# Kernel optimization log

Measured on AMD Instinct MI355X. Metric: run time of the kernel, lower is better.

Reference implementation:

```python
import jax, jax.numpy as jnp
import numpy as np

DIM = 1024
NQ = 16
NKV = 4
HD = DIM // NQ  # 64
HID = 2048
E = 8
B, S = 1, 1024
EPS = 1e-6


def rmsnorm(x, w):
    ms = jnp.mean(x * x, axis=-1, keepdims=True)
    return w * (x * jax.lax.rsqrt(ms + EPS))


def rope_tables(seq_len, head_dim):
    inv_freq = 1.0 / (10000.0 ** (jnp.arange(0, head_dim, 2, dtype=jnp.float32) / head_dim))
    t = jnp.arange(seq_len, dtype=jnp.float32)
    freqs = jnp.einsum('i,j->ij', t, inv_freq)  # [S, HD/2]
    return jnp.cos(freqs), jnp.sin(freqs)


def apply_rope(x, cos, sin):
    # x: [B, S, H, HD]; cos/sin: [S, HD/2]
    c = cos[None, :, None, :]
    s = sin[None, :, None, :]
    half = x.shape[-1] // 2
    x1, x2 = x[..., :half], x[..., half:]
    return jnp.concatenate([x1 * c - x2 * s, x1 * s + x2 * c], axis=-1)


def setup_inputs() -> dict:
    key = jax.random.key(0)
    ks = jax.random.split(key, 20)
    sc = lambda fan_in: 1.0 / np.sqrt(fan_in)
    d = {}
    d['x'] = jax.random.normal(ks[0], (B, S, DIM), dtype=jnp.float32)
    d['ln1_w'] = jnp.ones((DIM,), jnp.float32)
    d['ln2_w'] = jnp.ones((DIM,), jnp.float32)
    d['Wq'] = jax.random.normal(ks[1], (DIM, DIM), jnp.float32) * sc(DIM)
    d['bq'] = jnp.zeros((DIM,), jnp.float32)
    d['Wk'] = jax.random.normal(ks[2], (DIM, HD * NKV), jnp.float32) * sc(DIM)
    d['bk'] = jnp.zeros((HD * NKV,), jnp.float32)
    d['Wv'] = jax.random.normal(ks[3], (DIM, HD * NKV), jnp.float32) * sc(DIM)
    d['bv'] = jnp.zeros((HD * NKV,), jnp.float32)
    d['qn_w'] = jnp.ones((HD,), jnp.float32)
    d['kn_w'] = jnp.ones((HD,), jnp.float32)
    d['Wg'] = jax.random.normal(ks[4], (HD, HD), jnp.float32) * sc(HD)
    d['bg'] = jnp.zeros((HD,), jnp.float32)
    d['Wo'] = jax.random.normal(ks[5], (DIM, DIM), jnp.float32) * sc(DIM)
    d['bo'] = jnp.zeros((DIM,), jnp.float32)
    d['Wr'] = jax.random.normal(ks[6], (DIM, E), jnp.float32) * sc(DIM)
    d['br'] = jnp.zeros((E,), jnp.float32)
    d['W1'] = jax.random.normal(ks[7], (E, DIM, 2 * HID), jnp.float32) * sc(DIM)
    d['b1'] = jnp.zeros((E, 2 * HID), jnp.float32)
    d['W2'] = jax.random.normal(ks[8], (E, HID, DIM), jnp.float32) * sc(HID)
    d['b2'] = jnp.zeros((E, DIM), jnp.float32)
    return d


def _forward(x, ln1_w, ln2_w, Wq, bq, Wk, bk, Wv, bv, qn_w, kn_w, Wg, bg, Wo, bo,
             Wr, br, W1, b1, W2, b2):
    batch, seq, _ = x.shape
    cos, sin = rope_tables(seq, HD)

    # --- attention ---
    h = rmsnorm(x, ln1_w)
    q = (h @ Wq + bq).reshape(batch, seq, NQ, HD)
    k = (h @ Wk + bk).reshape(batch, seq, NKV, HD)
    v = (h @ Wv + bv).reshape(batch, seq, NKV, HD)
    q = rmsnorm(apply_rope(q, cos, sin), qn_w)
    k = rmsnorm(apply_rope(k, cos, sin), kn_w)
    rep = NQ // NKV
    k = jnp.repeat(k, rep, axis=2)  # [B,S,NQ,HD]
    v = jnp.repeat(v, rep, axis=2)
    scores = jnp.einsum('bthd,bshd->bhts', q, k) / np.sqrt(HD)
    causal = jnp.tril(jnp.ones((seq, seq), dtype=bool))
    scores = jnp.where(causal[None, None], scores, -jnp.inf)
    attn = jax.nn.softmax(scores, axis=-1)
    out = jnp.einsum('bhts,bshd->bthd', attn, v)
    gate = jax.nn.sigmoid(out @ Wg + bg)
    out = (out * gate).reshape(batch, seq, DIM)
    x = x + out @ Wo + bo

    # --- top-1 MoE (note: output is NOT scaled by router probs) ---
    h2 = rmsnorm(x, ln2_w)
    logits = h2 @ Wr + br  # [B,S,E]
    top1 = jnp.argmax(logits, axis=-1).reshape(-1)  # [T]
    xt = h2.reshape(-1, DIM)  # [T,DIM]
    # dense dispatch: run all experts, gather the chosen one
    u = jnp.einsum('td,edf->tef', xt, W1) + b1  # [T,E,2H]
    u1, u2 = u[..., :HID], u[..., HID:]
    act = u1 * jax.nn.sigmoid(u2)  # SwiGLU
    y_all = jnp.einsum('teh,ehd->ted', act, W2) + b2  # [T,E,DIM]
    y = jnp.take_along_axis(y_all, top1[:, None, None], axis=1)[:, 0, :]
    return x + y.reshape(batch, seq, DIM)


def reference(x, ln1_w, ln2_w, Wq, bq, Wk, bk, Wv, bv, qn_w, kn_w, Wg, bg, Wo, bo,
              Wr, br, W1, b1, W2, b2):
    return _forward(x, ln1_w, ln2_w, Wq, bq, Wk, bk, Wv, bv, qn_w, kn_w,
                    Wg, bg, Wo, bo, Wr, br, W1, b1, W2, b2)
```

## Files before the change

### kernel.cpp

```cpp
#include <hip/hip_runtime.h>
#include <hip/hip_bf16.h>
#include <cstddef>

#define DIM 1024
#define NQ 16
#define NKV 4
#define HD 64
#define HID 2048
#define NE 8
#define SEQ 1024
#define EPSF 1e-6f
#define MAX_TILES 24
#define GST 72

typedef __hip_bfloat16 bf16;
typedef __attribute__((ext_vector_type(8))) short short8;
typedef __attribute__((ext_vector_type(4))) float floatx4;

typedef union { short8 s; unsigned int u[4]; } s8u;

__device__ __forceinline__ unsigned int f2b(float f) {
    union { bf16 b; unsigned short s; } u;
    u.b = __float2bfloat16(f);
    return (unsigned int)u.s;
}
__device__ __forceinline__ unsigned int pk2(float a, float b) {
    return f2b(a) | (f2b(b) << 16);
}

__global__ __launch_bounds__(256) void rmsnorm_kernel(const float* __restrict__ src,
                                                      const float* __restrict__ w,
                                                      float* __restrict__ dst)
{
    int row = blockIdx.x, tid = threadIdx.x;
    __shared__ float red[256];
    float vals[4];
    float sq = 0.f;
    size_t base = (size_t)row * DIM;
    #pragma unroll
    for (int i = 0; i < 4; i++) {
        int idx = tid + i * 256;
        float v = src[base + idx];
        vals[i] = v; sq += v * v;
    }
    red[tid] = sq; __syncthreads();
    for (int s = 128; s > 0; s >>= 1) {
        if (tid < s) red[tid] += red[tid + s];
        __syncthreads();
    }
    float rs = 1.0f / sqrtf(red[0] * (1.0f / DIM) + EPSF);
    #pragma unroll
    for (int i = 0; i < 4; i++) {
        int idx = tid + i * 256;
        dst[base + idx] = w[idx] * vals[i] * rs;
    }
}

__global__ __launch_bounds__(256) void gemm_kernel(
    const float* __restrict__ A, const float* __restrict__ B, const float* __restrict__ bias,
    float* __restrict__ C, const float* __restrict__ resf,
    const int* __restrict__ perm, const int* __restrict__ tile_expert,
    int N, int K, int mode)
{
    __shared__ short As[64 * GST];
    __shared__ short Bs[64 * GST];
    int tid = threadIdx.x;
    int mbase = blockIdx.y * 64, nbase = blockIdx.x * 64;

    size_t Beoff = 0, biasoff = 0;
    if (tile_expert) {
        int e = tile_expert[blockIdx.y];
        if (e < 0) return;
        Beoff = (size_t)e * K * N;
        biasoff = (size_t)e * N;
    }

    int ar = tid >> 4, ak = (tid & 15) << 2;
    int bn = tid & 63, bkk = (tid >> 6) << 4;
    const float* BpBase = B + Beoff + (size_t)bkk * N + nbase + bn;

    int wv = tid >> 6, ln = tid & 63;
    int fm = (wv << 4) + (ln & 15);
    int fn = ln & 15;
    int fk = (ln >> 4) << 3;

    floatx4 acc[4];
    #pragma unroll
    for (int nt = 0; nt < 4; nt++)
        #pragma unroll
        for (int r = 0; r < 4; r++) acc[nt][r] = 0.f;

    for (int kt = 0; kt < K; kt += 64) {
        __syncthreads();
        #pragma unroll
        for (int p = 0; p < 4; p++) {
            int m = (p << 4) + ar;
            float4 v = *(const float4*)(A + (size_t)(mbase + m) * K + kt + ak);
            uint2 wpk; wpk.x = pk2(v.x, v.y); wpk.y = pk2(v.z, v.w);
            *(uint2*)&As[m * GST + ak] = wpk;
        }
        {
            const float* bp = BpBase + (size_t)kt * N;
            unsigned int u[8];
            #pragma unroll
            for (int i = 0; i < 8; i++)
                u[i] = pk2(bp[(size_t)(2 * i) * N], bp[(size_t)(2 * i + 1) * N]);
            *(uint4*)&Bs[bn * GST + bkk]     = make_uint4(u[0], u[1], u[2], u[3]);
            *(uint4*)&Bs[bn * GST + bkk + 8] = make_uint4(u[4], u[5], u[6], u[7]);
        }
        __syncthreads();
        #pragma unroll
        for (int ks = 0; ks < 2; ks++) {
            short8 af = *(const short8*)&As[fm * GST + (ks << 5) + fk];
            #pragma unroll
            for (int nt = 0; nt < 4; nt++) {
                short8 bf = *(const short8*)&Bs[((nt << 4) + fn) * GST + (ks << 5) + fk];
                acc[nt] = __builtin_amdgcn_mfma_f32_16x16x32_bf16(af, bf, acc[nt], 0, 0, 0);
            }
        }
    }

    int rowb = mbase + (wv << 4) + ((ln >> 4) << 2);
    if (mode == 2) {
        int tk[4];
        #pragma unroll
        for (int r = 0; r < 4; r++) tk[r] = perm[rowb + r];
        #pragma unroll
        for (int nt = 0; nt < 4; nt++) {
            int col = nbase + (nt << 4) + fn;
            float bsv = bias[biasoff + col];
            #pragma unroll
            for (int r = 0; r < 4; r++)
                if (tk[r] >= 0)
                    C[(size_t)tk[r] * N + col] = resf[(size_t)tk[r] * N + col] + acc[nt][r] + bsv;
        }
    } else {
        #pragma unroll
        for (int nt = 0; nt < 4; nt++) {
            int col = nbase + (nt << 4) + fn;
            float bsv = bias[col];
            #pragma unroll
            for (int r = 0; r < 4; r++) {
                float vv = acc[nt][r] + bsv;
                if (mode == 1) vv += resf[(size_t)(rowb + r) * N + col];
                C[(size_t)(rowb + r) * N + col] = vv;
            }
        }
    }
}

__global__ __launch_bounds__(256) void moe1_kernel(
    const float* __restrict__ A,
    const float* __restrict__ W1,
    const float* __restrict__ b1,
    float* __restrict__ act,
    const int* __restrict__ perm,
    const int* __restrict__ tile_expert)
{
    __shared__ short As[64 * GST];
    __shared__ short B1s[64 * GST];
    __shared__ short B2s[64 * GST];
    int tid = threadIdx.x;
    int mbase = blockIdx.y * 64, nbase = blockIdx.x * 64;
    int e = tile_expert[blockIdx.y];
    if (e < 0) return;
    const float* Wp = W1 + (size_t)e * DIM * (2 * HID);
    const float* bp1 = b1 + (size_t)e * (2 * HID);

    int ar = tid >> 4, ak = (tid & 15) << 2;
    int tok[4];
    #pragma unroll
    for (int p = 0; p < 4; p++) tok[p] = perm[mbase + (p << 4) + ar];

    int bn = tid & 63, bkk = (tid >> 6) << 4;
    const float* BpBase = Wp + (size_t)bkk * (2 * HID) + nbase + bn;

    int wv = tid >> 6, ln = tid & 63;
    int fm = (wv << 4) + (ln & 15);
    int fn = ln & 15;
    int fk = (ln >> 4) << 3;

    floatx4 acc1[4], acc2[4];
    #pragma unroll
    for (int nt = 0; nt < 4; nt++)
        #pragma unroll
        for (int r = 0; r < 4; r++) { acc1[nt][r] = 0.f; acc2[nt][r] = 0.f; }

    for (int kt = 0; kt < DIM; kt += 64) {
        __syncthreads();
        #pragma unroll
        for (int p = 0; p < 4; p++) {
            int m = (p << 4) + ar;
            float4 v = (tok[p] >= 0)
                ? *(const float4*)(A + (size_t)tok[p] * DIM + kt + ak)
                : make_float4(0.f, 0.f, 0.f, 0.f);
            uint2 wpk; wpk.x = pk2(v.x, v.y); wpk.y = pk2(v.z, v.w);
            *(uint2*)&As[m * GST + ak] = wpk;
        }
        {
            const float* bp = BpBase + (size_t)kt * (2 * HID);
            unsigned int u1[8], u2[8];
            #pragma unroll
            for (int i = 0; i < 8; i++) {
                u1[i] = pk2(bp[(size_t)(2 * i) * (2 * HID)],
                            bp[(size_t)(2 * i + 1) * (2 * HID)]);
                u2[i] = pk2(bp[(size_t)(2 * i) * (2 * HID) + HID],
                            bp[(size_t)(2 * i + 1) * (2 * HID) + HID]);
            }
            *(uint4*)&B1s[bn * GST + bkk]     = make_uint4(u1[0], u1[1], u1[2], u1[3]);
            *(uint4*)&B1s[bn * GST + bkk + 8] = make_uint4(u1[4], u1[5], u1[6], u1[7]);
            *(uint4*)&B2s[bn * GST + bkk]     = make_uint4(u2[0], u2[1], u2[2], u2[3]);
            *(uint4*)&B2s[bn * GST + bkk + 8] = make_uint4(u2[4], u2[5], u2[6], u2[7]);
        }
        __syncthreads();
        #pragma unroll
        for (int ks = 0; ks < 2; ks++) {
            short8 af = *(const short8*)&As[fm * GST + (ks << 5) + fk];
            #pragma unroll
            for (int nt = 0; nt < 4; nt++) {
                int bo = ((nt << 4) + fn) * GST + (ks << 5) + fk;
                short8 bf1 = *(const short8*)&B1s[bo];
                short8 bf2 = *(const short8*)&B2s[bo];
                acc1[nt] = __builtin_amdgcn_mfma_f32_16x16x32_bf16(af, bf1, acc1[nt], 0, 0, 0);
                acc2[nt] = __builtin_amdgcn_mfma_f32_16x16x32_bf16(af, bf2, acc2[nt], 0, 0, 0);
            }
        }
    }

    int rowb = mbase + (wv << 4) + ((ln >> 4) << 2);
    #pragma unroll
    for (int nt = 0; nt < 4; nt++) {
        int col = nbase + (nt << 4) + fn;
        float bs1 = bp1[col];
        float bs2 = bp1[HID + col];
        #pragma unroll
        for (int r = 0; r < 4; r++) {
            float u1 = acc1[nt][r] + bs1;
            float u2 = acc2[nt][r] + bs2;
            act[(size_t)(rowb + r) * HID + col] = u1 * (1.0f / (1.0f + expf(-u2)));
        }
    }
}

__global__ __launch_bounds__(64) void rope_rms_kernel(float* __restrict__ x,
                                                      const float* __restrict__ w, int nh)
{
    int t = blockIdx.x, h = blockIdx.y, d = threadIdx.x;
    int base = (t * nh + h) * HD;
    int i = d & 31;
    float x1 = x[base + i];
    float x2 = x[base + 32 + i];
    float inv = 1.0f / powf(10000.0f, (float)(2 * i) * (1.0f / HD));
    float fr = (float)t * inv;
    float c = cosf(fr), s = sinf(fr);
    float r = (d < 32) ? (x1 * c - x2 * s) : (x1 * s + x2 * c);
    float sq = r * r;
    #pragma unroll
    for (int m = 32; m >= 1; m >>= 1) sq += __shfl_xor(sq, m);
    float rs = 1.0f / sqrtf(sq * (1.0f / HD) + EPSF);
    __syncthreads();
    x[base + d] = r * rs * w[d];
}

__global__ __launch_bounds__(256) void fattn_kernel(const float* __restrict__ q,
                                                    const float* __restrict__ k,
                                                    const float* __restrict__ v,
                                                    float* __restrict__ o)
{
    __shared__ short lds[2][2][64 * GST];

    int h = blockIdx.x, qt = blockIdx.y;
    int kvh = h >> 2;
    int tid = threadIdx.x;
    int w = tid >> 6, ln = tid & 63;
    int c = ln & 15, g = ln >> 4;
    int qbase = qt * 64;
    const size_t krow = (size_t)NKV * HD;

    short8 qf[2];
    {
        const float* qp = q + ((size_t)(qbase + 16 * w + c) * NQ + h) * HD + 8 * g;
        #pragma unroll
        for (int ks = 0; ks < 2; ks++) {
            float4 a = *(const float4*)(qp + 32 * ks);
            float4 b = *(const float4*)(qp + 32 * ks + 4);
            s8u t;
            t.u[0] = pk2(a.x * 0.125f, a.y * 0.125f);
            t.u[1] = pk2(a.z * 0.125f, a.w * 0.125f);
            t.u[2] = pk2(b.x * 0.125f, b.y * 0.125f);
            t.u[3] = pk2(b.z * 0.125f, b.w * 0.125f);
            qf[ks] = t.s;
        }
    }

    int kr[4], kd4[4];
    #pragma unroll
    for (int i = 0; i < 4; i++) { int f4 = tid + 256 * i; kr[i] = f4 >> 4; kd4[i] = f4 & 15; }
    int vd = tid & 63, vrb = (tid >> 6) << 4;

    float4 kreg[4];
    float vreg[16];
    {
        const float* kb = k + (size_t)kvh * HD;
        #pragma unroll
        for (int i = 0; i < 4; i++)
            kreg[i] = *(const float4*)(kb + (size_t)kr[i] * krow + kd4[i] * 4);
        const float* vb = v + (size_t)kvh * HD + vd;
        #pragma unroll
        for (int i = 0; i < 16; i++)
            vreg[i] = vb[(size_t)(vrb + i) * krow];
    }

    float m_i = -INFINITY, l_i = 0.f;
    floatx4 ot[4];
    #pragma unroll
    for (int mt = 0; mt < 4; mt++)
        #pragma unroll
        for (int r = 0; r < 4; r++) ot[mt][r] = 0.f;

    for (int kt = 0; kt <= qt; kt++) {
        short* KB = lds[kt & 1][0];
        short* VT = lds[kt & 1][1];

        #pragma unroll
        for (int i = 0; i < 4; i++) {
            uint2 wp; wp.x = pk2(kreg[i].x, kreg[i].y); wp.y = pk2(kreg[i].z, kreg[i].w);
            *(uint2*)&KB[kr[i] * GST + kd4[i] * 4] = wp;
        }
        {
            unsigned int u[8];
            #pragma unroll
            for (int i = 0; i < 8; i++) u[i] = pk2(vreg[2 * i], vreg[2 * i + 1]);
            *(uint4*)&VT[vd * GST + vrb]     = make_uint4(u[0], u[1], u[2], u[3]);
            *(uint4*)&VT[vd * GST + vrb + 8] = make_uint4(u[4], u[5], u[6], u[7]);
        }
        __syncthreads();

        if (kt < qt) {
            int kb2 = (kt + 1) * 64;
            const float* kb = k + ((size_t)kb2 * NKV + kvh) * HD;
            #pragma unroll
            for (int i = 0; i < 4; i++)
                kreg[i] = *(const float4*)(kb + (size_t)kr[i] * krow + kd4[i] * 4);
            const float* vb = k == v ? nullptr : v;
            const float* vp = v + ((size_t)kb2 * NKV + kvh) * HD + vd;
            (void)vb;
            #pragma unroll
            for (int i = 0; i < 16; i++)
                vreg[i] = vp[(size_t)(vrb + i) * krow];
        }

        float p[4][4];
        #pragma unroll
        for (int mt = 0; mt < 4; mt++) {
            floatx4 s = {0.f, 0.f, 0.f, 0.f};
            #pragma unroll
            for (int ks = 0; ks < 2; ks++) {
                short8 kf = *(const short8*)&KB[(16 * mt + c) * GST + 32 * ks + 8 * g];
                s = __builtin_amdgcn_mfma_f32_16x16x32_bf16(kf, qf[ks], s, 0, 0, 0);
            }
            #pragma unroll
            for (int r = 0; r < 4; r++) p[mt][r] = s[r];
        }

        if (kt == qt) {
            #pragma unroll
            for (int mt = 0; mt < 4; mt++)
                #pragma unroll
                for (int r = 0; r < 4; r++)
                    if (16 * mt + 4 * g + r > 16 * w + c) p[mt][r] = -1e30f;
        }

        float tm = p[0][0];
        #pragma unroll
        for (int mt = 0; mt < 4; mt++)
            #pragma unroll
            for (int r = 0; r < 4; r++) tm = fmaxf(tm, p[mt][r]);
        tm = fmaxf(tm, __shfl_xor(tm, 16));
        tm = fmaxf(tm, __shfl_xor(tm, 32));
        float mn = fmaxf(m_i, tm);
        float alpha = __expf(m_i - mn);
        float ts = 0.f;
        #pragma unroll
        for (int mt = 0; mt < 4; mt++)
            #pragma unroll
            for (int r = 0; r < 4; r++) {
                float e = __expf(p[mt][r] - mn);
                p[mt][r] = e; ts += e;
            }
        ts += __shfl_xor(ts, 16);
        ts += __shfl_xor(ts, 32);
        l_i = alpha * l_i + ts;
        m_i = mn;
        #pragma unroll
        for (int mt = 0; mt < 4; mt++)
            #pragma unroll
            for (int r = 0; r < 4; r++) ot[mt][r] *= alpha;

        unsigned int pd[4][2];
        #pragma unroll
        for (int mt = 0; mt < 4; mt++) {
            pd[mt][0] = pk2(p[mt][0], p[mt][1]);
            pd[mt][1] = pk2(p[mt][2], p[mt][3]);
        }

        int srcA = c + ((ln & 16) << 1);
        int srcB = srcA + 16;
        int gh = g >> 1;
        short8 pf[2];
        #pragma unroll
        for (int ks = 0; ks < 2; ks++) {
            s8u t;
            unsigned int a0 = (unsigned)__shfl((int)pd[2 * ks][0],     srcA);
            unsigned int a1 = (unsigned)__shfl((int)pd[2 * ks + 1][0], srcA);
            t.u[0] = gh ? a1 : a0;
            unsigned int b0 = (unsigned)__shfl((int)pd[2 * ks][1],     srcA);
            unsigned int b1 = (unsigned)__shfl((int)pd[2 * ks + 1][1], srcA);
            t.u[1] = gh ? b1 : b0;
            unsigned int c0 = (unsigned)__shfl((int)pd[2 * ks][0],     srcB);
            unsigned int c1 = (unsigned)__shfl((int)pd[2 * ks + 1][0], srcB);
            t.u[2] = gh ? c1 : c0;
            unsigned int d0 = (unsigned)__shfl((int)pd[2 * ks][1],     srcB);
            unsigned int d1 = (unsigned)__shfl((int)pd[2 * ks + 1][1], srcB);
            t.u[3] = gh ? d1 : d0;
            pf[ks] = t.s;
        }

        #pragma unroll
        for (int mt = 0; mt < 4; mt++) {
            #pragma unroll
            for (int ks = 0; ks < 2; ks++) {
                short8 vf = *(const short8*)&VT[(16 * mt + c) * GST + 32 * ks + 8 * g];
                ot[mt] = __builtin_amdgcn_mfma_f32_16x16x32_bf16(vf, pf[ks], ot[mt], 0, 0, 0);
            }
        }
    }

    __syncthreads();
    float* OT = (float*)lds;
    float rl = 1.0f / l_i;
    #pragma unroll
    for (int mt = 0; mt < 4; mt++)
        #pragma unroll
        for (int r = 0; r < 4; r++)
            OT[(16 * w + c) * 68 + 16 * mt + 4 * g + r] = ot[mt][r] * rl;
    __syncthreads();
    #pragma unroll
    for (int i = 0; i < 4; i++) {
        int idx = tid + 256 * i;
        int rq = idx >> 4, d4 = idx & 15;
        float4 val = *(const float4*)&OT[rq * 68 + d4 * 4];
        *(float4*)(o + ((size_t)(qbase + rq) * NQ + h) * HD + d4 * 4) = val;
    }
}

__global__ __launch_bounds__(64) void gate_kernel(float* __restrict__ o,
                                                  const float* __restrict__ Wg,
                                                  const float* __restrict__ bg)
{
    int t = blockIdx.x, h = blockIdx.y, d = threadIdx.x;
    __shared__ float ao[HD];
    int base = (t * NQ + h) * HD;
    ao[d] = o[base + d];
    __syncthreads();
    float acc = bg[d];
    #pragma unroll 8
    for (int e = 0; e < HD; e++) acc += ao[e] * Wg[e * HD + d];
    float g = 1.0f / (1.0f + expf(-acc));
    o[base + d] = ao[d] * g;
}

__global__ __launch_bounds__(64) void router_kernel(const float* __restrict__ h2,
                                                    const float* __restrict__ Wr,
                                                    const float* __restrict__ br,
                                                    int* __restrict__ top1)
{
    int t = blockIdx.x, lane = threadIdx.x;
    float acc[NE] = {0.f, 0.f, 0.f, 0.f, 0.f, 0.f, 0.f, 0.f};
    for (int d = lane; d < DIM; d += 64) {
        float hv = h2[(size_t)t * DIM + d];
        float4 w0 = *(const float4*)(Wr + (size_t)d * NE);
        float4 w1 = *(const float4*)(Wr + (size_t)d * NE + 4);
        acc[0] += hv * w0.x; acc[1] += hv * w0.y;
        acc[2] += hv * w0.z; acc[3] += hv * w0.w;
        acc[4] += hv * w1.x; acc[5] += hv * w1.y;
        acc[6] += hv * w1.z; acc[7] += hv * w1.w;
    }
    #pragma unroll
    for (int e = 0; e < NE; e++)
        for (int off = 32; off >= 1; off >>= 1) acc[e] += __shfl_down(acc[e], off);
    if (lane == 0) {
        float best = acc[0] + br[0]; int be = 0;
        #pragma unroll
        for (int e = 1; e < NE; e++) {
            float l = acc[e] + br[e];
            if (l > best) { best = l; be = e; }
        }
        top1[t] = be;
    }
}

__global__ __launch_bounds__(64) void bucket_kernel(const int* __restrict__ top1,
                                                    int* __restrict__ perm,
                                                    int* __restrict__ tile_expert)
{
    int lane = threadIdx.x;

    int e_of[16];
    {
        const int4* tp = (const int4*)(top1 + lane * 16);
        #pragma unroll
        for (int c = 0; c < 4; c++) {
            int4 v = tp[c];
            e_of[c * 4 + 0] = v.x & 7;
            e_of[c * 4 + 1] = v.y & 7;
            e_of[c * 4 + 2] = v.z & 7;
            e_of[c * 4 + 3] = v.w & 7;
        }
    }

    int cnt[NE];
    #pragma unroll
    for (int e = 0; e < NE; e++) {
        int c = 0;
        #pragma unroll
        for (int i = 0; i < 16; i++) c += (e_of[i] == e) ? 1 : 0;
        cnt[e] = c;
    }

    int pre[NE];
    #pragma unroll
    for (int e = 0; e < NE; e++) pre[e] = cnt[e];
    #pragma unroll
    for (int off = 1; off < 64; off <<= 1) {
        #pragma unroll
        for (int e = 0; e < NE; e++) {
            int t = __shfl_up(pre[e], off);
            if (lane >= off) pre[e] += t;
        }
    }
    int tot[NE];
    #pragma unroll
    for (int e = 0; e < NE; e++) {
        tot[e] = __shfl(pre[e], 63);
        pre[e] -= cnt[e];
    }

    int off_e[NE + 1];
    off_e[0] = 0;
    #pragma unroll
    for (int e = 0; e < NE; e++)
        off_e[e + 1] = off_e[e] + (((tot[e] + 63) >> 6) << 6);

    if (lane < MAX_TILES) {
        int tb = lane << 6;
        int te = -1;
        #pragma unroll
        for (int e = 0; e < NE; e++)
            if (tb >= off_e[e] && tb < off_e[e + 1]) te = e;
        tile_expert[lane] = te;
    }

    #pragma unroll
    for (int e = 0; e < NE; e++)
        for (int i = off_e[e] + tot[e] + lane; i < off_e[e + 1]; i += 64)
            perm[i] = -1;

    #pragma unroll
    for (int e = 0; e < NE; e++) {
        int pos = off_e[e] + pre[e];
        #pragma unroll
        for (int i = 0; i < 16; i++) {
            if (e_of[i] == e) { perm[pos] = lane * 16 + i; pos++; }
        }
    }
}

extern "C" void kernel_launch(void* const* d_in, const int* in_sizes, int n_in,
                              void* d_out, int out_size, void* d_ws, size_t ws_size,
                              hipStream_t stream)
{
    const float* x    = (const float*)d_in[0];
    const float* ln1w = (const float*)d_in[1];
    const float* ln2w = (const float*)d_in[2];
    const float* Wq   = (const float*)d_in[3];
    const float* bq   = (const float*)d_in[4];
    const float* Wk   = (const float*)d_in[5];
    const float* bk   = (const float*)d_in[6];
    const float* Wv   = (const float*)d_in[7];
    const float* bv   = (const float*)d_in[8];
    const float* qnw  = (const float*)d_in[9];
    const float* knw  = (const float*)d_in[10];
    const float* Wg   = (const float*)d_in[11];
    const float* bg   = (const float*)d_in[12];
    const float* Wo   = (const float*)d_in[13];
    const float* bo   = (const float*)d_in[14];
    const float* Wr   = (const float*)d_in[15];
    const float* br   = (const float*)d_in[16];
    const float* W1   = (const float*)d_in[17];
    const float* b1   = (const float*)d_in[18];
    const float* W2   = (const float*)d_in[19];
    const float* b2   = (const float*)d_in[20];
    float* out = (float*)d_out;
    (void)in_sizes; (void)n_in; (void)out_size; (void)ws_size;

    char* ws = (char*)d_ws;
    float* h    = (float*)(ws);
    float* q    = (float*)(ws + ((size_t)4  << 20));
    float* kbuf = (float*)(ws + ((size_t)8  << 20));
    float* vbuf = (float*)(ws + ((size_t)9  << 20));
    float* ao   = (float*)(ws + ((size_t)10 << 20));
    float* x2   = (float*)(ws);
    float* h2   = (float*)(ws + ((size_t)4  << 20));
    float* act  = (float*)(ws + ((size_t)8  << 20));
    int* top1   = (int*)  (ws + ((size_t)20 << 20));
    int* perm   = top1 + 2048;
    int* texp   = perm + MAX_TILES * 64;

    rmsnorm_kernel<<<SEQ, 256, 0, stream>>>(x, ln1w, h);
    gemm_kernel<<<dim3(DIM / 64, SEQ / 64), 256, 0, stream>>>(
        h, Wq, bq, q, nullptr, nullptr, nullptr, DIM, DIM, 0);
    gemm_kernel<<<dim3((NKV * HD) / 64, SEQ / 64), 256, 0, stream>>>(
        h, Wk, bk, kbuf, nullptr, nullptr, nullptr, NKV * HD, DIM, 0);
    gemm_kernel<<<dim3((NKV * HD) / 64, SEQ / 64), 256, 0, stream>>>(
        h, Wv, bv, vbuf, nullptr, nullptr, nullptr, NKV * HD, DIM, 0);
    rope_rms_kernel<<<dim3(SEQ, NQ),  64, 0, stream>>>(q,    qnw, NQ);
    rope_rms_kernel<<<dim3(SEQ, NKV), 64, 0, stream>>>(kbuf, knw, NKV);
    fattn_kernel<<<dim3(NQ, SEQ / 64), 256, 0, stream>>>(q, kbuf, vbuf, ao);
    gate_kernel<<<dim3(SEQ, NQ), 64, 0, stream>>>(ao, Wg, bg);
    gemm_kernel<<<dim3(DIM / 64, SEQ / 64), 256, 0, stream>>>(
        ao, Wo, bo, x2, x, nullptr, nullptr, DIM, DIM, 1);
    rmsnorm_kernel<<<SEQ, 256, 0, stream>>>(x2, ln2w, h2);
    router_kernel<<<SEQ, 64, 0, stream>>>(h2, Wr, br, top1);
    bucket_kernel<<<1, 64, 0, stream>>>(top1, perm, texp);
    moe1_kernel<<<dim3(HID / 64, MAX_TILES), 256, 0, stream>>>(
        h2, W1, b1, act, perm, texp);
    gemm_kernel<<<dim3(DIM / 64, MAX_TILES), 256, 0, stream>>>(
        act, W2, b2, out, x2, perm, texp, DIM, HID, 2);
}
```

Baseline: 495.7 us.

## Prefetch next K-tile into registers in GEMMs and fuse QKV projections

The generic GEMM and the MoE first-layer kernel now load the next 64-wide K slice of A and B into registers while MFMAs run on the current slice in shared memory, so global-load latency overlaps with compute. The barrier is moved to the end of each iteration. The three separate Q, K and V projection launches are merged into one qkv_kernel with 24 column blocks that choose their weight matrix by block index, which cuts launch overhead and fills more of the GPU in a single grid. The cost is higher register pressure from the prefetch buffers (32 extra floats per thread in moe1), which may lower occupancy.

```diff
diff --git a/kernel.cpp b/kernel.cpp
--- a/kernel.cpp
+++ b/kernel.cpp
@@ -90,25 +90,41 @@
         #pragma unroll
         for (int r = 0; r < 4; r++) acc[nt][r] = 0.f;
 
+    float4 apre[4];
+    float bpre[16];
+    #pragma unroll
+    for (int p = 0; p < 4; p++)
+        apre[p] = *(const float4*)(A + (size_t)(mbase + (p << 4) + ar) * K + ak);
+    #pragma unroll
+    for (int i = 0; i < 16; i++)
+        bpre[i] = BpBase[(size_t)i * N];
+
     for (int kt = 0; kt < K; kt += 64) {
-        __syncthreads();
         #pragma unroll
         for (int p = 0; p < 4; p++) {
             int m = (p << 4) + ar;
-            float4 v = *(const float4*)(A + (size_t)(mbase + m) * K + kt + ak);
-            uint2 wpk; wpk.x = pk2(v.x, v.y); wpk.y = pk2(v.z, v.w);
+            uint2 wpk; wpk.x = pk2(apre[p].x, apre[p].y); wpk.y = pk2(apre[p].z, apre[p].w);
             *(uint2*)&As[m * GST + ak] = wpk;
         }
         {
-            const float* bp = BpBase + (size_t)kt * N;
             unsigned int u[8];
             #pragma unroll
-            for (int i = 0; i < 8; i++)
-                u[i] = pk2(bp[(size_t)(2 * i) * N], bp[(size_t)(2 * i + 1) * N]);
+            for (int i = 0; i < 8; i++) u[i] = pk2(bpre[2 * i], bpre[2 * i + 1]);
             *(uint4*)&Bs[bn * GST + bkk]     = make_uint4(u[0], u[1], u[2], u[3]);
             *(uint4*)&Bs[bn * GST + bkk + 8] = make_uint4(u[4], u[5], u[6], u[7]);
         }
         __syncthreads();
+
+        int kn = kt + 64;
+        if (kn < K) {
+            #pragma unroll
+            for (int p = 0; p < 4; p++)
+                apre[p] = *(const float4*)(A + (size_t)(mbase + (p << 4) + ar) * K + kn + ak);
+            const float* bp = BpBase + (size_t)kn * N;
+            #pragma unroll
+            for (int i = 0; i < 16; i++) bpre[i] = bp[(size_t)i * N];
+        }
+
         #pragma unroll
         for (int ks = 0; ks < 2; ks++) {
             short8 af = *(const short8*)&As[fm * GST + (ks << 5) + fk];
@@ -118,6 +134,7 @@
                 acc[nt] = __builtin_amdgcn_mfma_f32_16x16x32_bf16(af, bf, acc[nt], 0, 0, 0);
             }
         }
+        __syncthreads();
     }
 
     int rowb = mbase + (wv << 4) + ((ln >> 4) << 2);
@@ -146,6 +163,97 @@
                 C[(size_t)(rowb + r) * N + col] = vv;
             }
         }
+    }
+}
+
+__global__ __launch_bounds__(256) void qkv_kernel(
+    const float* __restrict__ A,
+    const float* __restrict__ Wq, const float* __restrict__ bq,
+    const float* __restrict__ Wk, const float* __restrict__ bk,
+    const float* __restrict__ Wv, const float* __restrict__ bv,
+    float* __restrict__ qo, float* __restrict__ ko, float* __restrict__ vo)
+{
+    __shared__ short As[64 * GST];
+    __shared__ short Bs[64 * GST];
+    int tid = threadIdx.x;
+    int bx = blockIdx.x;
+    int mbase = blockIdx.y * 64;
+
+    const float* B; const float* bias; float* C; int N, nbase;
+    if (bx < 16)      { B = Wq; bias = bq; C = qo; N = DIM;      nbase = bx * 64; }
+    else if (bx < 20) { B = Wk; bias = bk; C = ko; N = NKV * HD; nbase = (bx - 16) * 64; }
+    else              { B = Wv; bias = bv; C = vo; N = NKV * HD; nbase = (bx - 20) * 64; }
+
+    int ar = tid >> 4, ak = (tid & 15) << 2;
+    int bn = tid & 63, bkk = (tid >> 6) << 4;
+    const float* BpBase = B + (size_t)bkk * N + nbase + bn;
+
+    int wv = tid >> 6, ln = tid & 63;
+    int fm = (wv << 4) + (ln & 15);
+    int fn = ln & 15;
+    int fk = (ln >> 4) << 3;
+
+    floatx4 acc[4];
+    #pragma unroll
+    for (int nt = 0; nt < 4; nt++)
+        #pragma unroll
+        for (int r = 0; r < 4; r++) acc[nt][r] = 0.f;
+
+    float4 apre[4];
+    float bpre[16];
+    #pragma unroll
+    for (int p = 0; p < 4; p++)
+        apre[p] = *(const float4*)(A + (size_t)(mbase + (p << 4) + ar) * DIM + ak);
+    #pragma unroll
+    for (int i = 0; i < 16; i++)
+        bpre[i] = BpBase[(size_t)i * N];
+
+    for (int kt = 0; kt < DIM; kt += 64) {
+        #pragma unroll
+        for (int p = 0; p < 4; p++) {
+            int m = (p << 4) + ar;
+            uint2 wpk; wpk.x = pk2(apre[p].x, apre[p].y); wpk.y = pk2(apre[p].z, apre[p].w);
+            *(uint2*)&As[m * GST + ak] = wpk;
+        }
+        {
+            unsigned int u[8];
+            #pragma unroll
+            for (int i = 0; i < 8; i++) u[i] = pk2(bpre[2 * i], bpre[2 * i + 1]);
+            *(uint4*)&Bs[bn * GST + bkk]     = make_uint4(u[0], u[1], u[2], u[3]);
+            *(uint4*)&Bs[bn * GST + bkk + 8] = make_uint4(u[4], u[5], u[6], u[7]);
+        }
+        __syncthreads();
+
+        int kn = kt + 64;
+        if (kn < DIM) {
+            #pragma unroll
+            for (int p = 0; p < 4; p++)
+                apre[p] = *(const float4*)(A + (size_t)(mbase + (p << 4) + ar) * DIM + kn + ak);
+            const float* bp = BpBase + (size_t)kn * N;
+            #pragma unroll
+            for (int i = 0; i < 16; i++) bpre[i] = bp[(size_t)i * N];
+        }
+
+        #pragma unroll
+        for (int ks = 0; ks < 2; ks++) {
+            short8 af = *(const short8*)&As[fm * GST + (ks << 5) + fk];
+            #pragma unroll
+            for (int nt = 0; nt < 4; nt++) {
+                short8 bf = *(const short8*)&Bs[((nt << 4) + fn) * GST + (ks << 5) + fk];
+                acc[nt] = __builtin_amdgcn_mfma_f32_16x16x32_bf16(af, bf, acc[nt], 0, 0, 0);
+            }
+        }
+        __syncthreads();
+    }
+
+    int rowb = mbase + (wv << 4) + ((ln >> 4) << 2);
+    #pragma unroll
+    for (int nt = 0; nt < 4; nt++) {
+        int col = nbase + (nt << 4) + fn;
+        float bsv = bias[col];
+        #pragma unroll
+        for (int r = 0; r < 4; r++)
+            C[(size_t)(rowb + r) * N + col] = acc[nt][r] + bsv;
     }
 }
 
@@ -186,26 +294,32 @@
         #pragma unroll
         for (int r = 0; r < 4; r++) { acc1[nt][r] = 0.f; acc2[nt][r] = 0.f; }
 
+    float4 apre[4];
+    float b1pre[16], b2pre[16];
+    #pragma unroll
+    for (int p = 0; p < 4; p++)
+        apre[p] = (tok[p] >= 0)
+            ? *(const float4*)(A + (size_t)tok[p] * DIM + ak)
+            : make_float4(0.f, 0.f, 0.f, 0.f);
+    #pragma unroll
+    for (int i = 0; i < 16; i++) {
+        b1pre[i] = BpBase[(size_t)i * (2 * HID)];
+        b2pre[i] = BpBase[(size_t)i * (2 * HID) + HID];
+    }
+
     for (int kt = 0; kt < DIM; kt += 64) {
-        __syncthreads();
         #pragma unroll
         for (int p = 0; p < 4; p++) {
             int m = (p << 4) + ar;
-            float4 v = (tok[p] >= 0)
-                ? *(const float4*)(A + (size_t)tok[p] * DIM + kt + ak)
-                : make_float4(0.f, 0.f, 0.f, 0.f);
-            uint2 wpk; wpk.x = pk2(v.x, v.y); wpk.y = pk2(v.z, v.w);
+            uint2 wpk; wpk.x = pk2(apre[p].x, apre[p].y); wpk.y = pk2(apre[p].z, apre[p].w);
             *(uint2*)&As[m * GST + ak] = wpk;
         }
         {
-            const float* bp = BpBase + (size_t)kt * (2 * HID);
             unsigned int u1[8], u2[8];
             #pragma unroll
             for (int i = 0; i < 8; i++) {
-                u1[i] = pk2(bp[(size_t)(2 * i) * (2 * HID)],
-                            bp[(size_t)(2 * i + 1) * (2 * HID)]);
-                u2[i] = pk2(bp[(size_t)(2 * i) * (2 * HID) + HID],
-                            bp[(size_t)(2 * i + 1) * (2 * HID) + HID]);
+                u1[i] = pk2(b1pre[2 * i], b1pre[2 * i + 1]);
+                u2[i] = pk2(b2pre[2 * i], b2pre[2 * i + 1]);
             }
             *(uint4*)&B1s[bn * GST + bkk]     = make_uint4(u1[0], u1[1], u1[2], u1[3]);
             *(uint4*)&B1s[bn * GST + bkk + 8] = make_uint4(u1[4], u1[5], u1[6], u1[7]);
@@ -213,6 +327,22 @@
             *(uint4*)&B2s[bn * GST + bkk + 8] = make_uint4(u2[4], u2[5], u2[6], u2[7]);
         }
         __syncthreads();
+
+        int kn = kt + 64;
+        if (kn < DIM) {
+            #pragma unroll
+            for (int p = 0; p < 4; p++)
+                apre[p] = (tok[p] >= 0)
+                    ? *(const float4*)(A + (size_t)tok[p] * DIM + kn + ak)
+                    : make_float4(0.f, 0.f, 0.f, 0.f);
+            const float* bp = BpBase + (size_t)kn * (2 * HID);
+            #pragma unroll
+            for (int i = 0; i < 16; i++) {
+                b1pre[i] = bp[(size_t)i * (2 * HID)];
+                b2pre[i] = bp[(size_t)i * (2 * HID) + HID];
+            }
+        }
+
         #pragma unroll
         for (int ks = 0; ks < 2; ks++) {
             short8 af = *(const short8*)&As[fm * GST + (ks << 5) + fk];
@@ -225,6 +355,7 @@
                 acc2[nt] = __builtin_amdgcn_mfma_f32_16x16x32_bf16(af, bf2, acc2[nt], 0, 0, 0);
             }
         }
+        __syncthreads();
     }
 
     int rowb = mbase + (wv << 4) + ((ln >> 4) << 2);
@@ -342,9 +473,7 @@
             #pragma unroll
             for (int i = 0; i < 4; i++)
                 kreg[i] = *(const float4*)(kb + (size_t)kr[i] * krow + kd4[i] * 4);
-            const float* vb = k == v ? nullptr : v;
             const float* vp = v + ((size_t)kb2 * NKV + kvh) * HD + vd;
-            (void)vb;
             #pragma unroll
             for (int i = 0; i < 16; i++)
                 vreg[i] = vp[(size_t)(vrb + i) * krow];
@@ -618,12 +747,8 @@
     int* texp   = perm + MAX_TILES * 64;
 
     rmsnorm_kernel<<<SEQ, 256, 0, stream>>>(x, ln1w, h);
-    gemm_kernel<<<dim3(DIM / 64, SEQ / 64), 256, 0, stream>>>(
-        h, Wq, bq, q, nullptr, nullptr, nullptr, DIM, DIM, 0);
-    gemm_kernel<<<dim3((NKV * HD) / 64, SEQ / 64), 256, 0, stream>>>(
-        h, Wk, bk, kbuf, nullptr, nullptr, nullptr, NKV * HD, DIM, 0);
-    gemm_kernel<<<dim3((NKV * HD) / 64, SEQ / 64), 256, 0, stream>>>(
-        h, Wv, bv, vbuf, nullptr, nullptr, nullptr, NKV * HD, DIM, 0);
+    qkv_kernel<<<dim3(24, SEQ / 64), 256, 0, stream>>>(
+        h, Wq, bq, Wk, bk, Wv, bv, q, kbuf, vbuf);
     rope_rms_kernel<<<dim3(SEQ, NQ),  64, 0, stream>>>(q,    qnw, NQ);
     rope_rms_kernel<<<dim3(SEQ, NKV), 64, 0, stream>>>(kbuf, knw, NKV);
     fattn_kernel<<<dim3(NQ, SEQ / 64), 256, 0, stream>>>(q, kbuf, vbuf, ao);
```

Measured after the change: 436.9 us. 1.13x faster.
